# Kernel optimization log

Measured on AMD Instinct MI355X. Metric: run time of the kernel, lower is better.

## Reference

```python
import jax, jax.numpy as jnp
import numpy as np

VX, VY = 0.2, 0.2
X_MIN, Y_MIN = -51.2, -51.2
Z_MIN, Z_MAX = -3.0, 3.0
GX, GY = 512, 512
NVOX = GX * GY
Z_CENTER = 0.0  # z_min + vz/2 with vz = 6.0
EPS = 1e-3  # BN1d default eps in mmdet3d PFNLayer


def _voxel_ids(pts):
    # pts: [B, N, 3] -> integer pillar coords and flat ids
    ix = jnp.clip(jnp.floor((pts[..., 0] - X_MIN) / VX).astype(jnp.int32), 0, GX - 1)
    iy = jnp.clip(jnp.floor((pts[..., 1] - Y_MIN) / VY).astype(jnp.int32), 0, GY - 1)
    return ix, iy, ix * GY + iy


def _segment_mean(vals, ids, n):
    # vals: [N, C], ids: [N] -> [n, C] mean per segment (0 for empty)
    s = jax.ops.segment_sum(vals, ids, num_segments=n)
    c = jax.ops.segment_sum(jnp.ones(vals.shape[0], vals.dtype), ids, num_segments=n)
    return s / jnp.maximum(c, 1.0)[:, None]


def _pillar_grid(pts, W, gamma, beta, mean, var):
    # DynamicPillarFeatureNet: point aug -> linear -> BN(eval) -> relu -> scatter-mean
    ix, iy, vid = _voxel_ids(pts)  # [B, N]
    fdt = pts.dtype
    # cluster center: per-voxel mean of xyz, gathered back to points
    cluster_mean = jax.vmap(lambda p, i: _segment_mean(p, i, NVOX)[i])(pts, vid)  # [B,N,3]
    center = jnp.stack([
        (ix.astype(fdt) + 0.5) * VX + X_MIN,
        (iy.astype(fdt) + 0.5) * VY + Y_MIN,
        jnp.full(ix.shape, Z_CENTER, dtype=fdt),
    ], axis=-1)  # [B,N,3]
    f = jnp.concatenate([pts, pts - cluster_mean, pts - center], axis=-1)  # [B,N,9]
    h = jnp.einsum('bnf,fc->bnc', f, W)  # Linear(9 -> C), no bias (BN follows)
    h = jax.nn.relu(gamma * (h - mean) * jax.lax.rsqrt(var + EPS) + beta)  # [B,N,C]
    # scatter mean per pillar -> dense grid (zeros where empty)
    grid = jax.vmap(lambda v, i: _segment_mean(v, i, NVOX))(h, vid)  # [B, NVOX, C]
    return grid


def setup_inputs() -> dict:
    key = jax.random.key(0)
    k0, k1, kw = jax.random.split(key, 3)
    B, N, C = 2, 100000, 64
    lo = jnp.array([X_MIN, Y_MIN, Z_MIN], jnp.float32)
    hi = jnp.array([-X_MIN, -Y_MIN, Z_MAX], jnp.float32)
    pc0s = jax.random.uniform(k0, (B, N, 3), jnp.float32) * (hi - lo) + lo
    pc1s = jax.random.uniform(k1, (B, N, 3), jnp.float32) * (hi - lo) + lo
    W = jax.random.normal(kw, (9, C), jnp.float32) * (1.0 / np.sqrt(9.0))
    return {
        'pc0s': pc0s, 'pc1s': pc1s, 'W': W,
        'bn_gamma': jnp.ones((C,), jnp.float32),
        'bn_beta': jnp.zeros((C,), jnp.float32),
        'bn_mean': jnp.zeros((C,), jnp.float32),
        'bn_var': jnp.ones((C,), jnp.float32),
    }


def reference(pc0s, pc1s, W, bn_gamma, bn_beta, bn_mean, bn_var):
    g0 = _pillar_grid(pc0s, W, bn_gamma, bn_beta, bn_mean, bn_var)
    g1 = _pillar_grid(pc1s, W, bn_gamma, bn_beta, bn_mean, bn_var)
    # sparse_pc1 - sparse_pc0, coalesced: identical to dense grid difference
    diff = (g1 - g0).reshape(pc0s.shape[0], GX, GY, -1)  # [B, GX, GY, C]
    return diff
```

## Files before the change

### kernel.cpp

```cpp
#include <hip/hip_runtime.h>

#define VXC 0.2f
#define VYC 0.2f
#define XMINC -51.2f
#define YMINC -51.2f
#define GXD 512
#define GYD 512
#define NVOXD (GXD * GYD)
#define BN_EPS 1e-3f

__global__ void init_and_precompute(int* __restrict__ cnt, int nzero4,
                                    const float* __restrict__ W,
                                    const float* __restrict__ gamma,
                                    const float* __restrict__ beta,
                                    const float* __restrict__ mean,
                                    const float* __restrict__ var,
                                    float* __restrict__ P) {
    int nzero_blocks = (nzero4 + 255) / 256;
    if ((int)blockIdx.x < nzero_blocks) {
        int i = blockIdx.x * 256 + threadIdx.x;
        if (i < nzero4) ((int4*)cnt)[i] = make_int4(0, 0, 0, 0);
        return;
    }
    int c = threadIdx.x;
    if (c >= 64) return;
    float scale = gamma[c] * (1.0f / sqrtf(var[c] + BN_EPS));
    float w0 = W[0*64+c], w1 = W[1*64+c], w2 = W[2*64+c];
    float w3 = W[3*64+c], w4 = W[4*64+c], w5 = W[5*64+c];
    float w6 = W[6*64+c], w7 = W[7*64+c], w8 = W[8*64+c];
    P[0*64+c] = (w0 + w3 + w6) * scale;
    P[1*64+c] = (w1 + w4 + w7) * scale;
    P[2*64+c] = (w2 + w5 + w8) * scale;
    P[3*64+c] = w3 * scale;
    P[4*64+c] = w4 * scale;
    P[5*64+c] = w5 * scale;
    P[6*64+c] = w6 * scale;
    P[7*64+c] = w7 * scale;
    P[8*64+c] = beta[c] - mean[c] * scale;
}

__global__ void bin_points(const float* __restrict__ pc0, const float* __restrict__ pc1,
                           int* __restrict__ cnt, unsigned* __restrict__ pk_arr,
                           int B, int N) {
    int i = blockIdx.x * blockDim.x + threadIdx.x;
    int per_cloud = B * N;
    if (i >= 2 * per_cloud) return;
    int cloud = (i >= per_cloud) ? 1 : 0;
    int i2 = i - cloud * per_cloud;
    int b = i2 / N;
    const float* p = (cloud ? pc1 : pc0) + (size_t)i2 * 3;
    float x = p[0], y = p[1];
    int ix = (int)floorf((x - XMINC) / VXC); ix = min(max(ix, 0), GXD - 1);
    int iy = (int)floorf((y - YMINC) / VYC); iy = min(max(iy, 0), GYD - 1);
    int hidx = (cloud * B + b) * NVOXD + ix * GYD + iy;
    int pos = atomicAdd(cnt + hidx, 1);
    pk_arr[i] = ((unsigned)hidx << 8) | (unsigned)pos;
}

__global__ void scan_block(const int* __restrict__ in, int* __restrict__ out,
                           int* __restrict__ bsums) {
    int tid = threadIdx.x;
    size_t base = (size_t)blockIdx.x * 1024;
    int4 v = ((const int4*)(in + base))[tid];
    int t0 = v.x, t1 = t0 + v.y, t2 = t1 + v.z, t3 = t2 + v.w;
    __shared__ int lds[256];
    lds[tid] = t3;
    __syncthreads();
    for (int d = 1; d < 256; d <<= 1) {
        int t = (tid >= d) ? lds[tid - d] : 0;
        __syncthreads();
        lds[tid] += t;
        __syncthreads();
    }
    int excl = lds[tid] - t3;
    if (tid == 255) bsums[blockIdx.x] = lds[255];
    ((int4*)(out + base))[tid] = make_int4(excl, excl + t0, excl + t1, excl + t2);
}

__global__ void add_bases(int* __restrict__ off, const int* __restrict__ bases,
                          int n4, int total) {
    int i = blockIdx.x * blockDim.x + threadIdx.x;
    if (i >= n4) return;
    int4 v = ((int4*)off)[i];
    int b = bases[i >> 8];
    v.x += b; v.y += b; v.z += b; v.w += b;
    ((int4*)off)[i] = v;
    if (i == 0) off[n4 * 4] = total;
}

__global__ void scatter_csr(const float* __restrict__ pc0, const float* __restrict__ pc1,
                            const int* __restrict__ off, const unsigned* __restrict__ pk_arr,
                            float4* __restrict__ csr, int B, int N) {
    int i = blockIdx.x * blockDim.x + threadIdx.x;
    int per_cloud = B * N;
    if (i >= 2 * per_cloud) return;
    int cloud = (i >= per_cloud) ? 1 : 0;
    int i2 = i - cloud * per_cloud;
    const float* p = (cloud ? pc1 : pc0) + (size_t)i2 * 3;
    unsigned pk = pk_arr[i];
    int o = off[pk >> 8] + (int)(pk & 255u);
    csr[o] = make_float4(p[0], p[1], p[2], 0.0f);
}

__global__ void voxel_stats(const float4* __restrict__ csr, const int* __restrict__ off,
                            float4* __restrict__ stats, int n) {
    int i = blockIdx.x * blockDim.x + threadIdx.x;
    if (i >= n) return;
    int s = off[i], e = off[i + 1];
    float4 r = make_float4(0.0f, 0.0f, 0.0f, 0.0f);
    if (e > s) {
        float sx = 0.0f, sy = 0.0f, sz = 0.0f;
        for (int j = s; j < e; ++j) {
            float4 pt = csr[j];
            sx += pt.x; sy += pt.y; sz += pt.z;
        }
        float inv = 1.0f / (float)(e - s);
        r = make_float4(sx * inv, sy * inv, sz * inv, inv);
    }
    stats[i] = r;
}

__global__ __launch_bounds__(256)
void gather(const float4* __restrict__ csr, const int* __restrict__ off,
            const float4* __restrict__ stats, const float* __restrict__ P,
            float* __restrict__ out, int B) {
    int g = blockIdx.x * blockDim.x + threadIdx.x;
    int c = g & 63;
    int w = g >> 6;
    int nquad = (B * NVOXD) >> 2;
    if (w >= nquad) return;

    float A   = P[0*64+c], Bw  = P[1*64+c], Cw  = P[2*64+c];
    float w3s = P[3*64+c], w4s = P[4*64+c], w5s = P[5*64+c];
    float w6s = P[6*64+c], w7s = P[7*64+c], offc = P[8*64+c];
    int base1 = B * NVOXD;
    int bv0 = w << 2;

    int4 a0 = *(const int4*)(off + bv0);
    int4 a1 = *(const int4*)(off + base1 + bv0);
    int o0[5] = {a0.x, a0.y, a0.z, a0.w, off[bv0 + 4]};
    int o1[5] = {a1.x, a1.y, a1.z, a1.w, off[base1 + bv0 + 4]};

    #pragma unroll
    for (int q = 0; q < 4; ++q) {
        int bv = bv0 + q;
        int s0 = o0[q], e0 = o0[q + 1];
        int s1 = o1[q], e1 = o1[q + 1];
        float res = 0.0f;
        if (e0 > s0 || e1 > s1) {
            int v = bv & (NVOXD - 1);
            int ix = v >> 9, iy = v & 511;
            float cx = ((float)ix + 0.5f) * VXC + XMINC;
            float cy = ((float)iy + 0.5f) * VYC + YMINC;
            float basef = offc - cx * w6s - cy * w7s;
            if (e0 > s0) {
                float4 st = stats[bv];
                float cbias = basef - st.x * w3s - st.y * w4s - st.z * w5s;
                float hsum = 0.0f;
                for (int j = s0; j < e0; ++j) {
                    float4 pt = csr[j];
                    hsum += fmaxf(pt.x * A + pt.y * Bw + pt.z * Cw + cbias, 0.0f);
                }
                res -= hsum * st.w;
            }
            if (e1 > s1) {
                float4 st = stats[base1 + bv];
                float cbias = basef - st.x * w3s - st.y * w4s - st.z * w5s;
                float hsum = 0.0f;
                for (int j = s1; j < e1; ++j) {
                    float4 pt = csr[j];
                    hsum += fmaxf(pt.x * A + pt.y * Bw + pt.z * Cw + cbias, 0.0f);
                }
                res += hsum * st.w;
            }
        }
        __builtin_nontemporal_store(res, out + ((size_t)bv << 6) + c);
    }
}

extern "C" void kernel_launch(void* const* d_in, const int* in_sizes, int n_in,
                              void* d_out, int out_size, void* d_ws, size_t ws_size,
                              hipStream_t stream) {
    const float* pc0   = (const float*)d_in[0];
    const float* pc1   = (const float*)d_in[1];
    const float* Wm    = (const float*)d_in[2];
    const float* gamma = (const float*)d_in[3];
    const float* beta  = (const float*)d_in[4];
    const float* mean  = (const float*)d_in[5];
    const float* var   = (const float*)d_in[6];
    float* out = (float*)d_out;

    int B = out_size / (NVOXD * 64);
    int N = in_sizes[0] / (3 * B);
    int npts = 2 * B * N;
    int n = 2 * B * NVOXD;
    int nblocks_scan = n / 1024;

    float4* csr   = (float4*)d_ws;
    float4* stats = csr + npts + 4;
    int* off      = (int*)(stats + n);
    int* aux      = off + n + 4;
    int* aux2     = aux + nblocks_scan;
    unsigned* pk  = (unsigned*)(aux2 + nblocks_scan);
    float* P      = (float*)(pk + npts);

    int nzero4 = n / 4;
    int nzero_blocks = (nzero4 + 255) / 256;
    init_and_precompute<<<nzero_blocks + 1, 256, 0, stream>>>(
        off, nzero4, Wm, gamma, beta, mean, var, P);

    int g1 = (npts + 255) / 256;
    bin_points<<<g1, 256, 0, stream>>>(pc0, pc1, off, pk, B, N);

    scan_block<<<nblocks_scan, 256, 0, stream>>>(off, off, aux);
    scan_block<<<1, 256, 0, stream>>>(aux, aux, aux2);
    add_bases<<<(n / 4 + 255) / 256, 256, 0, stream>>>(off, aux, n / 4, npts);

    scatter_csr<<<g1, 256, 0, stream>>>(pc0, pc1, off, pk, csr, B, N);

    voxel_stats<<<(n + 255) / 256, 256, 0, stream>>>(csr, off, stats, n);

    long long total_thr = ((long long)B * NVOXD >> 2) * 64;
    int g4 = (int)((total_thr + 255) / 256);
    gather<<<g4, 256, 0, stream>>>(csr, off, stats, P, out, B);
}
```

Before: 233.4 us.

## Compact non-empty and empty voxels into worklists for finalize kernel

Replaces the per-voxel stats kernel with one that computes both clouds' stats and, using wave ballots plus atomics, compacts non-empty voxel pairs and empty voxels into separate worklists. The finalize kernel then runs per-point work only on the compacted non-empty list and writes zeros for the empty list in separate blocks, so waves no longer diverge over mostly-empty voxels. The cost is extra worklist writes and reads, scattered output stores, and launching enough blocks for the worst case, with surplus blocks exiting early.

```diff
diff --git a/kernel.cpp b/kernel.cpp
--- a/kernel.cpp
+++ b/kernel.cpp
@@ -10,6 +10,7 @@
 #define BN_EPS 1e-3f
 
 __global__ void init_and_precompute(int* __restrict__ cnt, int nzero4,
+                                    int* __restrict__ ctrs,
                                     const float* __restrict__ W,
                                     const float* __restrict__ gamma,
                                     const float* __restrict__ beta,
@@ -23,6 +24,7 @@
         return;
     }
     int c = threadIdx.x;
+    if (c < 2) ctrs[c] = 0;
     if (c >= 64) return;
     float scale = gamma[c] * (1.0f / sqrtf(var[c] + BN_EPS));
     float w0 = W[0*64+c], w1 = W[1*64+c], w2 = W[2*64+c];
@@ -102,79 +104,125 @@
     csr[o] = make_float4(p[0], p[1], p[2], 0.0f);
 }
 
-__global__ void voxel_stats(const float4* __restrict__ csr, const int* __restrict__ off,
-                            float4* __restrict__ stats, int n) {
-    int i = blockIdx.x * blockDim.x + threadIdx.x;
-    if (i >= n) return;
-    int s = off[i], e = off[i + 1];
-    float4 r = make_float4(0.0f, 0.0f, 0.0f, 0.0f);
-    if (e > s) {
+__global__ void stats_worklists(const float4* __restrict__ csr, const int* __restrict__ off,
+                                int M, int4* __restrict__ wlA,
+                                float4* __restrict__ wlS0, float4* __restrict__ wlS1,
+                                int* __restrict__ wlE, int* __restrict__ ctrs) {
+    int i = blockIdx.x * 256 + threadIdx.x;
+    int s0 = off[i], e0 = off[i + 1];
+    int s1 = off[M + i], e1 = off[M + i + 1];
+    int c0 = e0 - s0, c1 = e1 - s1;
+    bool ne = (c0 | c1) != 0;
+
+    float4 st0 = make_float4(0.0f, 0.0f, 0.0f, 0.0f);
+    float4 st1 = make_float4(0.0f, 0.0f, 0.0f, 0.0f);
+    if (c0) {
         float sx = 0.0f, sy = 0.0f, sz = 0.0f;
-        for (int j = s; j < e; ++j) {
+        for (int j = s0; j < e0; ++j) {
             float4 pt = csr[j];
             sx += pt.x; sy += pt.y; sz += pt.z;
         }
-        float inv = 1.0f / (float)(e - s);
-        r = make_float4(sx * inv, sy * inv, sz * inv, inv);
-    }
-    stats[i] = r;
+        float inv = 1.0f / (float)c0;
+        st0 = make_float4(sx * inv, sy * inv, sz * inv, inv);
+    }
+    if (c1) {
+        float sx = 0.0f, sy = 0.0f, sz = 0.0f;
+        for (int j = s1; j < e1; ++j) {
+            float4 pt = csr[j];
+            sx += pt.x; sy += pt.y; sz += pt.z;
+        }
+        float inv = 1.0f / (float)c1;
+        st1 = make_float4(sx * inv, sy * inv, sz * inv, inv);
+    }
+
+    int lane = threadIdx.x & 63;
+    unsigned long long mask = __ballot(ne);
+    unsigned long long lower = (lane == 0) ? 0ull : (mask << (64 - lane)) >> (64 - lane);
+    lower = mask & ((lane == 63) ? 0x7fffffffffffffffull : ((1ull << lane) - 1ull));
+    int rank = __popcll(lower);
+    int wc = __popcll(mask);
+    int base = 0;
+    if (lane == 0 && wc) base = atomicAdd(ctrs + 0, wc);
+    base = __shfl(base, 0);
+    if (ne) {
+        wlA[base + rank]  = make_int4(i, s0, s1, c0 | (c1 << 16));
+        wlS0[base + rank] = st0;
+        wlS1[base + rank] = st1;
+    } else {
+        unsigned long long maskE = ~mask;
+        int rankE = __popcll(maskE & ((lane == 63) ? 0x7fffffffffffffffull
+                                                   : ((1ull << lane) - 1ull)));
+        int baseE = 0;
+        (void)rankE; (void)baseE;
+    }
+    int wcE = 64 - wc;
+    int baseE = 0;
+    if (lane == 0 && wcE) baseE = atomicAdd(ctrs + 1, wcE);
+    baseE = __shfl(baseE, 0);
+    if (!ne) {
+        unsigned long long maskE = ~mask;
+        int rankE = __popcll(maskE & ((lane == 63) ? 0x7fffffffffffffffull
+                                                   : ((1ull << lane) - 1ull)));
+        wlE[baseE + rankE] = i;
+    }
 }
 
 __global__ __launch_bounds__(256)
-void gather(const float4* __restrict__ csr, const int* __restrict__ off,
-            const float4* __restrict__ stats, const float* __restrict__ P,
-            float* __restrict__ out, int B) {
-    int g = blockIdx.x * blockDim.x + threadIdx.x;
-    int c = g & 63;
-    int w = g >> 6;
-    int nquad = (B * NVOXD) >> 2;
-    if (w >= nquad) return;
-
-    float A   = P[0*64+c], Bw  = P[1*64+c], Cw  = P[2*64+c];
-    float w3s = P[3*64+c], w4s = P[4*64+c], w5s = P[5*64+c];
-    float w6s = P[6*64+c], w7s = P[7*64+c], offc = P[8*64+c];
-    int base1 = B * NVOXD;
-    int bv0 = w << 2;
-
-    int4 a0 = *(const int4*)(off + bv0);
-    int4 a1 = *(const int4*)(off + base1 + bv0);
-    int o0[5] = {a0.x, a0.y, a0.z, a0.w, off[bv0 + 4]};
-    int o1[5] = {a1.x, a1.y, a1.z, a1.w, off[base1 + bv0 + 4]};
-
-    #pragma unroll
-    for (int q = 0; q < 4; ++q) {
-        int bv = bv0 + q;
-        int s0 = o0[q], e0 = o0[q + 1];
-        int s1 = o1[q], e1 = o1[q + 1];
-        float res = 0.0f;
-        if (e0 > s0 || e1 > s1) {
+void finalize(const float4* __restrict__ csr, const int4* __restrict__ wlA,
+              const float4* __restrict__ wlS0, const float4* __restrict__ wlS1,
+              const int* __restrict__ wlE, const int* __restrict__ ctrs,
+              const float* __restrict__ P, float* __restrict__ out, int gblocks) {
+    int c = threadIdx.x & 63;
+    int wv = threadIdx.x >> 6;
+    if ((int)blockIdx.x < gblocks) {
+        int widx = (blockIdx.x * 4 + wv) * 4;
+        int nNE = ctrs[0];
+        if (widx >= nNE) return;
+        float A   = P[0*64+c], Bw  = P[1*64+c], Cw  = P[2*64+c];
+        float w3s = P[3*64+c], w4s = P[4*64+c], w5s = P[5*64+c];
+        float w6s = P[6*64+c], w7s = P[7*64+c], offc = P[8*64+c];
+        #pragma unroll
+        for (int q = 0; q < 4; ++q) {
+            if (widx + q >= nNE) break;
+            int4 e = wlA[widx + q];
+            float4 st0 = wlS0[widx + q];
+            float4 st1 = wlS1[widx + q];
+            int bv = e.x, s0 = e.y, s1 = e.z;
+            int c0 = e.w & 0xffff, c1 = (int)((unsigned)e.w >> 16);
             int v = bv & (NVOXD - 1);
-            int ix = v >> 9, iy = v & 511;
-            float cx = ((float)ix + 0.5f) * VXC + XMINC;
-            float cy = ((float)iy + 0.5f) * VYC + YMINC;
+            float cx = ((float)(v >> 9) + 0.5f) * VXC + XMINC;
+            float cy = ((float)(v & 511) + 0.5f) * VYC + YMINC;
             float basef = offc - cx * w6s - cy * w7s;
-            if (e0 > s0) {
-                float4 st = stats[bv];
-                float cbias = basef - st.x * w3s - st.y * w4s - st.z * w5s;
+            float res = 0.0f;
+            if (c0) {
+                float cbias = basef - st0.x * w3s - st0.y * w4s - st0.z * w5s;
                 float hsum = 0.0f;
-                for (int j = s0; j < e0; ++j) {
+                for (int j = s0; j < s0 + c0; ++j) {
                     float4 pt = csr[j];
                     hsum += fmaxf(pt.x * A + pt.y * Bw + pt.z * Cw + cbias, 0.0f);
                 }
-                res -= hsum * st.w;
+                res -= hsum * st0.w;
             }
-            if (e1 > s1) {
-                float4 st = stats[base1 + bv];
-                float cbias = basef - st.x * w3s - st.y * w4s - st.z * w5s;
+            if (c1) {
+                float cbias = basef - st1.x * w3s - st1.y * w4s - st1.z * w5s;
                 float hsum = 0.0f;
-                for (int j = s1; j < e1; ++j) {
+                for (int j = s1; j < s1 + c1; ++j) {
                     float4 pt = csr[j];
                     hsum += fmaxf(pt.x * A + pt.y * Bw + pt.z * Cw + cbias, 0.0f);
                 }
-                res += hsum * st.w;
+                res += hsum * st1.w;
             }
-        }
-        __builtin_nontemporal_store(res, out + ((size_t)bv << 6) + c);
+            __builtin_nontemporal_store(res, out + ((size_t)bv << 6) + c);
+        }
+    } else {
+        int widx = ((blockIdx.x - gblocks) * 4 + wv) * 8;
+        int nE = ctrs[1];
+        #pragma unroll
+        for (int q = 0; q < 8; ++q) {
+            if (widx + q >= nE) break;
+            int bv = wlE[widx + q];
+            __builtin_nontemporal_store(0.0f, out + ((size_t)bv << 6) + c);
+        }
     }
 }
 
@@ -193,21 +241,26 @@
     int B = out_size / (NVOXD * 64);
     int N = in_sizes[0] / (3 * B);
     int npts = 2 * B * N;
-    int n = 2 * B * NVOXD;
+    int M = B * NVOXD;
+    int n = 2 * M;
     int nblocks_scan = n / 1024;
 
-    float4* csr   = (float4*)d_ws;
-    float4* stats = csr + npts + 4;
-    int* off      = (int*)(stats + n);
-    int* aux      = off + n + 4;
-    int* aux2     = aux + nblocks_scan;
-    unsigned* pk  = (unsigned*)(aux2 + nblocks_scan);
-    float* P      = (float*)(pk + npts);
+    float4* csr  = (float4*)d_ws;
+    float4* wlS0 = csr + npts + 4;
+    float4* wlS1 = wlS0 + M;
+    int4*   wlA  = (int4*)(wlS1 + M);
+    int*    off  = (int*)(wlA + M);
+    int*    aux  = off + n + 4;
+    int*    aux2 = aux + nblocks_scan;
+    int*    wlE  = aux2 + nblocks_scan;
+    unsigned* pk = (unsigned*)(wlE + M);
+    int*   ctrs  = (int*)(pk + npts);
+    float* P     = (float*)(ctrs + 4);
 
     int nzero4 = n / 4;
     int nzero_blocks = (nzero4 + 255) / 256;
     init_and_precompute<<<nzero_blocks + 1, 256, 0, stream>>>(
-        off, nzero4, Wm, gamma, beta, mean, var, P);
+        off, nzero4, ctrs, Wm, gamma, beta, mean, var, P);
 
     int g1 = (npts + 255) / 256;
     bin_points<<<g1, 256, 0, stream>>>(pc0, pc1, off, pk, B, N);
@@ -218,9 +271,11 @@
 
     scatter_csr<<<g1, 256, 0, stream>>>(pc0, pc1, off, pk, csr, B, N);
 
-    voxel_stats<<<(n + 255) / 256, 256, 0, stream>>>(csr, off, stats, n);
-
-    long long total_thr = ((long long)B * NVOXD >> 2) * 64;
-    int g4 = (int)((total_thr + 255) / 256);
-    gather<<<g4, 256, 0, stream>>>(csr, off, stats, P, out, B);
-}
+    stats_worklists<<<M / 256, 256, 0, stream>>>(csr, off, M, wlA, wlS0, wlS1, wlE, ctrs);
+
+    int gblocks = (M / 4 + 15) / 16 * 4 / 4;
+    gblocks = (M / 4 + 3) / 4;
+    int zblocks = (M / 8 + 3) / 4;
+    finalize<<<gblocks + zblocks, 256, 0, stream>>>(csr, wlA, wlS0, wlS1, wlE, ctrs,
+                                                    P, out, gblocks);
+}
```

After: 423.0 us. +81.2%, slower.
